# Kernel optimization log

Hardware: AMD Instinct MI355X
Metric: run time of the kernel (lower is better)

## Reference

```python
import jax, jax.numpy as jnp
import numpy as np

N = 100_000      # nodes
E = 1_600_000    # edges (avg degree 16)
IN, H, OUT = 128, 64, 32
G = 128          # graphs in batch
EPS = 1e-5


def setup_inputs() -> dict:
    key = jax.random.key(0)
    ks = jax.random.split(key, 12)
    x = jax.random.normal(ks[0], (N, IN), jnp.float32)
    edge_index = jax.random.randint(ks[1], (2, E), 0, N, dtype=jnp.int32)
    batch = jnp.sort(jax.random.randint(ks[2], (N,), 0, G, dtype=jnp.int32))
    # GCNConv weights (glorot-ish scaling), shared BatchNorm params, final linear
    W1 = jax.random.normal(ks[3], (IN, H), jnp.float32) / np.sqrt(IN)
    b1 = jnp.zeros((H,), jnp.float32)
    W2 = jax.random.normal(ks[4], (H, H), jnp.float32) / np.sqrt(H)
    b2 = jnp.zeros((H,), jnp.float32)
    gamma = jnp.ones((H,), jnp.float32)
    beta = jnp.zeros((H,), jnp.float32)
    linW = jax.random.normal(ks[5], (H, OUT), jnp.float32) / np.sqrt(H)
    linb = jnp.zeros((OUT,), jnp.float32)
    return dict(x=x, edge_index=edge_index, batch=batch, W1=W1, b1=b1,
                W2=W2, b2=b2, gamma=gamma, beta=beta, linW=linW, linb=linb)


def _gcn_edges(edge_index):
    # add self loops (PyG GCNConv default) and symmetric normalization
    loop = jnp.arange(N, dtype=edge_index.dtype)
    src = jnp.concatenate([edge_index[0], loop])
    dst = jnp.concatenate([edge_index[1], loop])
    deg = jax.ops.segment_sum(jnp.ones_like(src, jnp.float32), dst, num_segments=N)
    dis = jnp.where(deg > 0, jax.lax.rsqrt(deg), 0.0)
    norm = dis[src] * dis[dst]          # [E+N]
    return src, dst, norm


def _gcn_conv(h, W, b, src, dst, norm):
    h = h @ W                            # [N, out] small GEMM first (PyG order)
    msg = h[src] * norm[:, None]         # gather + edgewise normalize
    return jax.ops.segment_sum(msg, dst, num_segments=N) + b  # scatter-add


def _batchnorm(h, gamma, beta):
    # training-mode batch stats over nodes (biased variance, as torch BN)
    mean = h.mean(axis=0)
    var = jnp.mean((h - mean) ** 2, axis=0)
    return (h - mean) * jax.lax.rsqrt(var + EPS) * gamma + beta


def reference(x, edge_index, batch, W1, b1, W2, b2, gamma, beta, linW, linb):
    src, dst, norm = _gcn_edges(edge_index)
    h = jax.nn.relu(_batchnorm(_gcn_conv(x, W1, b1, src, dst, norm), gamma, beta))
    h = jax.nn.relu(_batchnorm(_gcn_conv(h, W2, b2, src, dst, norm), gamma, beta))
    # global mean pool over graph ids
    sums = jax.ops.segment_sum(h, batch, num_segments=G)
    cnts = jax.ops.segment_sum(jnp.ones((N,), h.dtype), batch, num_segments=G)
    pooled = sums / jnp.maximum(cnts, 1.0)[:, None]   # [G, H]
    return pooled @ linW + linb                        # [G, OUT]
```

## Files before the change

kernel.cpp:

```cpp
#include <hip/hip_runtime.h>

#define NNODES 100000
#define NEDGES 1600000
#define FIN 128
#define FH 64
#define FOUT 32
#define NGRAPH 128
#define EPSV 1e-5f

#define NBLK ((NNODES + 255) / 256)
#define GM ((NNODES + 63) / 64)
#define FILLBLK 2048
#define POOL_WAVES 1024

typedef unsigned short ushort_t;
typedef __attribute__((ext_vector_type(8))) short bf16x8;
typedef __attribute__((ext_vector_type(4))) float f32x4;

__device__ inline unsigned f2bf(float f) {
  union { float f; unsigned u; } x;
  x.f = f;
  return (x.u + 0x7fffu + ((x.u >> 16) & 1u)) >> 16;
}
__device__ inline float bflo(unsigned u) {
  union { unsigned u; float f; } x;
  x.u = u << 16;
  return x.f;
}
__device__ inline float bfhi(unsigned u) {
  union { unsigned u; float f; } x;
  x.u = u & 0xffff0000u;
  return x.f;
}


__global__ void k_deg_accum(const int* __restrict__ dst, int* __restrict__ deg) {
  const int SLICE = NNODES / 8;
  int xcd = blockIdx.x & 7;
  int lo = xcd * SLICE, hi = lo + SLICE;
  int chunk = blockIdx.x >> 3;
  int nchunk = gridDim.x >> 3;
  for (int i = chunk * blockDim.x + threadIdx.x; i < NEDGES; i += nchunk * blockDim.x) {
    int d = dst[i];
    if (d >= lo && d < hi) atomicAdd(&deg[d], 1);
  }
}


__global__ void k_scan_atomic(const int* __restrict__ deg, int* __restrict__ gtotal,
                              int* __restrict__ off, float* __restrict__ dis) {
  __shared__ int ls[256];
  __shared__ int sbase;
  int b = blockIdx.x, t = threadIdx.x;
  int i = b * 256 + t;
  int v = (i < NNODES) ? deg[i] : 0;
  ls[t] = v;
  __syncthreads();
  for (int s = 1; s < 256; s <<= 1) {
    int add = (t >= s) ? ls[t - s] : 0;
    __syncthreads();
    ls[t] += add;
    __syncthreads();
  }
  if (t == 255) sbase = atomicAdd(gtotal, ls[255]);
  __syncthreads();
  if (i < NNODES) {
    off[i] = sbase + ls[t] - v;
    dis[i] = rsqrtf((float)v + 1.0f);
  }
}


template <int K, bool BN>
__device__ __forceinline__ void gemm_body(int bid, const float* __restrict__ A,
                                          const float* __restrict__ W,
                                          const float* __restrict__ stats,
                                          const float* __restrict__ gamma,
                                          const float* __restrict__ beta,
                                          const float* __restrict__ dis,
                                          ushort_t* __restrict__ out, ushort_t* wt,
                                          float* bn_sc, float* bn_sh) {
  const int WT = K + 8;
  if (BN && threadIdx.x < K) {
    int f = threadIdx.x;
    float mean = stats[f] * (1.0f / NNODES);
    float var = stats[K + f] * (1.0f / NNODES) - mean * mean;
    float s = gamma[f] * rsqrtf(var + EPSV);
    bn_sc[f] = s;
    bn_sh[f] = beta[f] - mean * s;
  }
  for (int idx = threadIdx.x; idx < K * 64; idx += 256) {
    int k = idx >> 6, col = idx & 63;
    wt[col * WT + k] = (ushort_t)f2bf(W[idx]);
  }
  __syncthreads();

  int wave = threadIdx.x >> 6;
  int lane = threadIdx.x & 63;
  int rrow = lane & 15;
  int g = lane >> 4;
  int row0 = (bid * 4 + wave) * 16;
  int arow = min(row0 + rrow, NNODES - 1);
  const float* a = A + (long long)arow * K;

  f32x4 acc0 = {0.f, 0.f, 0.f, 0.f}, acc1 = acc0, acc2 = acc0, acc3 = acc0;

#pragma unroll
  for (int ks = 0; ks < K / 32; ++ks) {
    int koff = ks * 32 + g * 8;
    f32x4 xa = __builtin_nontemporal_load((const f32x4*)(a + koff));
    f32x4 xb = __builtin_nontemporal_load((const f32x4*)(a + koff + 4));
    float xs[8] = {xa.x, xa.y, xa.z, xa.w, xb.x, xb.y, xb.z, xb.w};
    if (BN) {
#pragma unroll
      for (int j = 0; j < 8; ++j)
        xs[j] = fmaxf(fmaf(xs[j], bn_sc[koff + j], bn_sh[koff + j]), 0.0f);
    }
    bf16x8 af;
#pragma unroll
    for (int j = 0; j < 8; ++j) af[j] = (short)f2bf(xs[j]);
    bf16x8 b0 = *(const bf16x8*)&wt[(0 * 16 + rrow) * WT + koff];
    bf16x8 b1 = *(const bf16x8*)&wt[(1 * 16 + rrow) * WT + koff];
    bf16x8 b2 = *(const bf16x8*)&wt[(2 * 16 + rrow) * WT + koff];
    bf16x8 b3 = *(const bf16x8*)&wt[(3 * 16 + rrow) * WT + koff];
    acc0 = __builtin_amdgcn_mfma_f32_16x16x32_bf16(af, b0, acc0, 0, 0, 0);
    acc1 = __builtin_amdgcn_mfma_f32_16x16x32_bf16(af, b1, acc1, 0, 0, 0);
    acc2 = __builtin_amdgcn_mfma_f32_16x16x32_bf16(af, b2, acc2, 0, 0, 0);
    acc3 = __builtin_amdgcn_mfma_f32_16x16x32_bf16(af, b3, acc3, 0, 0, 0);
  }

  int orow0 = row0 + g * 4;
#pragma unroll
  for (int r = 0; r < 4; ++r) {
    int orow = orow0 + r;
    if (orow < NNODES) {
      float d = dis[orow];
      ushort_t* o = out + (long long)orow * FH + rrow;
      o[0] = (ushort_t)f2bf(acc0[r] * d);
      o[16] = (ushort_t)f2bf(acc1[r] * d);
      o[32] = (ushort_t)f2bf(acc2[r] * d);
      o[48] = (ushort_t)f2bf(acc3[r] * d);
    }
  }
}

template <int K, bool BN>
__global__ void k_gemm_mfma(const float* __restrict__ A, const float* __restrict__ W,
                            const float* __restrict__ stats, const float* __restrict__ gamma,
                            const float* __restrict__ beta, const float* __restrict__ dis,
                            ushort_t* __restrict__ out) {
  __shared__ ushort_t wt[64 * (K + 8)];
  __shared__ float sc[K], sh[K];
  gemm_body<K, BN>(blockIdx.x, A, W, stats, gamma, beta, dis, out, wt, sc, sh);
}


__global__ void k_fill_gemm1(const float* __restrict__ x, const float* __restrict__ W1,
                             const float* __restrict__ dis, ushort_t* __restrict__ bufA,
                             const int* __restrict__ src, const int* __restrict__ dst,
                             const int* __restrict__ off, int* __restrict__ cursor,
                             int* __restrict__ csr) {
  __shared__ ushort_t wt[64 * (FIN + 8)];
  if (blockIdx.x < GM) {
    gemm_body<FIN, false>(blockIdx.x, x, W1, nullptr, nullptr, nullptr, dis, bufA, wt,
                          nullptr, nullptr);
  } else {
    int bb = blockIdx.x - GM;
    const int SLICE = NNODES / 8;
    int xcd = bb & 7;
    int lo = xcd * SLICE, hi = lo + SLICE;
    int chunk = bb >> 3;
    int nchunk = FILLBLK >> 3;
    for (int i = chunk * blockDim.x + threadIdx.x; i < NEDGES; i += nchunk * blockDim.x) {
      int d = dst[i];
      if (d >= lo && d < hi) {
        int p = atomicAdd(&cursor[d], 1);
        csr[off[d] + p] = src[i];
      }
    }
  }
}


#define ACC8(acc, u, ok)                       \
  acc[0] += (ok) ? bflo(u.x) : 0.0f;           \
  acc[1] += (ok) ? bfhi(u.x) : 0.0f;           \
  acc[2] += (ok) ? bflo(u.y) : 0.0f;           \
  acc[3] += (ok) ? bfhi(u.y) : 0.0f;           \
  acc[4] += (ok) ? bflo(u.z) : 0.0f;           \
  acc[5] += (ok) ? bfhi(u.z) : 0.0f;           \
  acc[6] += (ok) ? bflo(u.w) : 0.0f;           \
  acc[7] += (ok) ? bfhi(u.w) : 0.0f;

__global__ void k_gather(const ushort_t* __restrict__ hs, const int* __restrict__ csr,
                         const int* __restrict__ off, const int* __restrict__ deg,
                         const float* __restrict__ dis, float* __restrict__ out,
                         float* __restrict__ stats) {
  __shared__ float ls[2 * FH];
  int tid = threadIdx.x;
  if (tid < 2 * FH) ls[tid] = 0.0f;
  __syncthreads();
  int lane = tid & 63;
  int q = lane >> 3;
  int i = lane & 7;
  int wid = (blockIdx.x * blockDim.x + tid) >> 6;
  int nw = (gridDim.x * blockDim.x) >> 6;
  const int HALF = NNODES / 2;
  float s1[8], s2[8];
#pragma unroll
  for (int f = 0; f < 8; ++f) s1[f] = s2[f] = 0.0f;

  for (int p = wid; p < HALF; p += nw) {
    int dA = p, dB = p + HALF;
    int bA = off[dA], eA = bA + deg[dA];
    int bB = off[dB], eB = bB + deg[dB];
    uint4 selfA = *(const uint4*)(hs + (long long)dA * FH + i * 8);
    uint4 selfB = *(const uint4*)(hs + (long long)dB * FH + i * 8);
    float accA[8], accB[8];
#pragma unroll
    for (int f = 0; f < 8; ++f) accA[f] = accB[f] = 0.0f;
    bool q0 = (q == 0);
    ACC8(accA, selfA, q0);
    ACC8(accB, selfB, q0);

    int nA = (eA - bA + 15) >> 4, nB = (eB - bB + 15) >> 4;
    int niter = max(nA, nB);
    int lastA = max(eA - 1, 0), lastB = max(eB - 1, 0);
    int kA0 = bA + q, kA1 = bA + q + 8;
    int kB0 = bB + q, kB1 = bB + q + 8;
    for (int j = 0; j < niter; ++j) {
      int a0 = kA0 + 16 * j, a1 = kA1 + 16 * j;
      int b0 = kB0 + 16 * j, b1 = kB1 + 16 * j;
      int cA0 = csr[min(a0, lastA)];
      int cA1 = csr[min(a1, lastA)];
      int cB0 = csr[min(b0, lastB)];
      int cB1 = csr[min(b1, lastB)];
      uint4 uA0 = *(const uint4*)(hs + (long long)cA0 * FH + i * 8);
      uint4 uA1 = *(const uint4*)(hs + (long long)cA1 * FH + i * 8);
      uint4 uB0 = *(const uint4*)(hs + (long long)cB0 * FH + i * 8);
      uint4 uB1 = *(const uint4*)(hs + (long long)cB1 * FH + i * 8);
      bool A0 = a0 < eA, A1 = a1 < eA, B0 = b0 < eB, B1 = b1 < eB;
      ACC8(accA, uA0, A0);
      ACC8(accA, uA1, A1);
      ACC8(accB, uB0, B0);
      ACC8(accB, uB1, B1);
    }
#pragma unroll
    for (int f = 0; f < 8; ++f) {
      accA[f] += __shfl_xor(accA[f], 8);
      accA[f] += __shfl_xor(accA[f], 16);
      accA[f] += __shfl_xor(accA[f], 32);
      accB[f] += __shfl_xor(accB[f], 8);
      accB[f] += __shfl_xor(accB[f], 16);
      accB[f] += __shfl_xor(accB[f], 32);
    }
    float ddA = dis[dA], ddB = dis[dB];
#pragma unroll
    for (int f = 0; f < 8; ++f) {
      accA[f] *= ddA;
      accB[f] *= ddB;
      s1[f] += accA[f] + accB[f];
      s2[f] += accA[f] * accA[f] + accB[f] * accB[f];
    }
    if (q == 0) {
      f32x4 v0 = {accA[0], accA[1], accA[2], accA[3]};
      f32x4 v1 = {accA[4], accA[5], accA[6], accA[7]};
      *(f32x4*)(out + (long long)dA * FH + i * 8) = v0;
      *(f32x4*)(out + (long long)dA * FH + i * 8 + 4) = v1;
    } else if (q == 1) {
      f32x4 v0 = {accB[0], accB[1], accB[2], accB[3]};
      f32x4 v1 = {accB[4], accB[5], accB[6], accB[7]};
      *(f32x4*)(out + (long long)dB * FH + i * 8) = v0;
      *(f32x4*)(out + (long long)dB * FH + i * 8 + 4) = v1;
    }
  }
  if (q == 2) {
#pragma unroll
    for (int f = 0; f < 8; ++f) {
      atomicAdd(&ls[i * 8 + f], s1[f]);
      atomicAdd(&ls[FH + i * 8 + f], s2[f]);
    }
  }
  __syncthreads();
  if (tid < 2 * FH) atomicAdd(&stats[tid], ls[tid]);
}


__global__ void k_pool(const float* __restrict__ h, const int* __restrict__ batch,
                       const float* __restrict__ stats, const float* __restrict__ gamma,
                       const float* __restrict__ beta, float* __restrict__ pooled,
                       float* __restrict__ cnt) {
  const int CHUNK = (NNODES + POOL_WAVES - 1) / POOL_WAVES;
  int lane = threadIdx.x & 63;
  int wid = (blockIdx.x * blockDim.x + threadIdx.x) >> 6;
  int start = wid * CHUNK;
  if (start >= NNODES) return;
  int end = min(start + CHUNK, NNODES);
  float mean = stats[lane] * (1.0f / NNODES);
  float var = stats[FH + lane] * (1.0f / NNODES) - mean * mean;
  float sc = gamma[lane] * rsqrtf(var + EPSV);
  float sh = beta[lane] - mean * sc;
  int cur = batch[start];
  float acc = 0.0f;
  int cl = 0;
  for (int n = start; n < end; ++n) {
    int g = batch[n];
    if (g != cur) {
      atomicAdd(&pooled[cur * FH + lane], acc);
      if (lane == 0) atomicAdd(&cnt[cur], (float)cl);
      acc = 0.0f;
      cl = 0;
      cur = g;
    }
    float v = fmaf(h[(long long)n * FH + lane], sc, sh);
    acc += fmaxf(v, 0.0f);
    ++cl;
  }
  atomicAdd(&pooled[cur * FH + lane], acc);
  if (lane == 0) atomicAdd(&cnt[cur], (float)cl);
}


__global__ void k_final(const float* __restrict__ pooled, const float* __restrict__ cnt,
                        const float* __restrict__ linW, const float* __restrict__ linb,
                        float* __restrict__ out) {
  int t = blockIdx.x * blockDim.x + threadIdx.x;
  if (t >= NGRAPH * FOUT) return;
  int g = t / FOUT, o = t % FOUT;
  float inv = 1.0f / fmaxf(cnt[g], 1.0f);
  float acc = linb[o];
#pragma unroll
  for (int k = 0; k < FH; ++k) acc = fmaf(pooled[g * FH + k] * inv, linW[k * FOUT + o], acc);
  out[t] = acc;
}

extern "C" void kernel_launch(void* const* d_in, const int* in_sizes, int n_in,
                              void* d_out, int out_size, void* d_ws, size_t ws_size,
                              hipStream_t stream) {
  const float* x = (const float*)d_in[0];
  const int* esrc = (const int*)d_in[1];
  const int* edst = (const int*)d_in[1] + NEDGES;
  const int* batch = (const int*)d_in[2];
  const float* W1 = (const float*)d_in[3];
  const float* W2 = (const float*)d_in[5];
  const float* gamma = (const float*)d_in[7];
  const float* beta = (const float*)d_in[8];
  const float* linW = (const float*)d_in[9];
  const float* linb = (const float*)d_in[10];
  float* out = (float*)d_out;

  ushort_t* bufA = (ushort_t*)d_ws;
  float* bufB = (float*)(bufA + (long long)NNODES * FH);
  float* dis = bufB + (long long)NNODES * FH;
  int* off = (int*)(dis + NNODES);
  int* csr = off + NNODES;
  int* deg = csr + NEDGES;
  int* cursor = deg + NNODES;
  int* gtotal = cursor + NNODES;
  float* stats1 = (float*)(gtotal + 1);
  float* stats2 = stats1 + 2 * FH;
  float* pooled = stats2 + 2 * FH;
  float* cnt = pooled + NGRAPH * FH;

  const int BT = 256;

  hipMemsetAsync(deg, 0,
                 (size_t)(2 * NNODES + 1 + 2 * 2 * FH + NGRAPH * FH + NGRAPH) * sizeof(int),
                 stream);

  k_deg_accum<<<2048, BT, 0, stream>>>(edst, deg);
  k_scan_atomic<<<NBLK, BT, 0, stream>>>(deg, gtotal, off, dis);
  k_fill_gemm1<<<GM + FILLBLK, BT, 0, stream>>>(x, W1, dis, bufA, esrc, edst, off, cursor, csr);

  k_gather<<<2048, BT, 0, stream>>>(bufA, csr, off, deg, dis, bufB, stats1);

  k_gemm_mfma<FH, true><<<GM, BT, 0, stream>>>(bufB, W2, stats1, gamma, beta, dis, bufA);
  k_gather<<<2048, BT, 0, stream>>>(bufA, csr, off, deg, dis, bufB, stats2);

  k_pool<<<POOL_WAVES * 64 / BT, BT, 0, stream>>>(bufB, batch, stats2, gamma, beta, pooled, cnt);
  k_final<<<(NGRAPH * FOUT + BT - 1) / BT, BT, 0, stream>>>(pooled, cnt, linW, linb, out);
}
```

Baseline: 432.0 us.

## Fuse mean pooling and final linear into one per-graph kernel

Replaces the atomic chunked pooling kernel and the separate final linear kernel with one kernel that launches one block per graph. Each block binary-searches the sorted batch array for its node range, reduces in shared memory and applies the linear layer. This removes one launch, the global atomics and part of the memset. The cost is only 128 blocks of 4 waves each, which may underuse the GPU while streaming the node features.

```diff
diff --git a/kernel.cpp b/kernel.cpp
--- a/kernel.cpp
+++ b/kernel.cpp
@@ -11,7 +11,6 @@
 #define NBLK ((NNODES + 255) / 256)
 #define GM ((NNODES + 63) / 64)
 #define FILLBLK 2048
-#define POOL_WAVES 1024
 
 typedef unsigned short ushort_t;
 typedef __attribute__((ext_vector_type(8))) short bf16x8;
@@ -286,52 +285,52 @@
 }
 
 
-__global__ void k_pool(const float* __restrict__ h, const int* __restrict__ batch,
-                       const float* __restrict__ stats, const float* __restrict__ gamma,
-                       const float* __restrict__ beta, float* __restrict__ pooled,
-                       float* __restrict__ cnt) {
-  const int CHUNK = (NNODES + POOL_WAVES - 1) / POOL_WAVES;
-  int lane = threadIdx.x & 63;
-  int wid = (blockIdx.x * blockDim.x + threadIdx.x) >> 6;
-  int start = wid * CHUNK;
-  if (start >= NNODES) return;
-  int end = min(start + CHUNK, NNODES);
+__global__ void k_pool_final(const float* __restrict__ h, const int* __restrict__ batch,
+                             const float* __restrict__ stats, const float* __restrict__ gamma,
+                             const float* __restrict__ beta, const float* __restrict__ linW,
+                             const float* __restrict__ linb, float* __restrict__ out) {
+  __shared__ int srange[2];
+  __shared__ float partial[4][FH];
+  __shared__ float pooledv[FH];
+  int g = blockIdx.x;
+  int tid = threadIdx.x;
+  if (tid < 2) {
+    int target = g + tid;
+    int lo = 0, hi = NNODES;
+    while (lo < hi) {
+      int mid = (lo + hi) >> 1;
+      if (batch[mid] < target) lo = mid + 1;
+      else hi = mid;
+    }
+    srange[tid] = lo;
+  }
+  __syncthreads();
+  int start = srange[0], end = srange[1];
+  int lane = tid & 63;
+  int wave = tid >> 6;
   float mean = stats[lane] * (1.0f / NNODES);
   float var = stats[FH + lane] * (1.0f / NNODES) - mean * mean;
   float sc = gamma[lane] * rsqrtf(var + EPSV);
   float sh = beta[lane] - mean * sc;
-  int cur = batch[start];
   float acc = 0.0f;
-  int cl = 0;
-  for (int n = start; n < end; ++n) {
-    int g = batch[n];
-    if (g != cur) {
-      atomicAdd(&pooled[cur * FH + lane], acc);
-      if (lane == 0) atomicAdd(&cnt[cur], (float)cl);
-      acc = 0.0f;
-      cl = 0;
-      cur = g;
-    }
+  for (int n = start + wave; n < end; n += 4) {
     float v = fmaf(h[(long long)n * FH + lane], sc, sh);
     acc += fmaxf(v, 0.0f);
-    ++cl;
-  }
-  atomicAdd(&pooled[cur * FH + lane], acc);
-  if (lane == 0) atomicAdd(&cnt[cur], (float)cl);
-}
-
-
-__global__ void k_final(const float* __restrict__ pooled, const float* __restrict__ cnt,
-                        const float* __restrict__ linW, const float* __restrict__ linb,
-                        float* __restrict__ out) {
-  int t = blockIdx.x * blockDim.x + threadIdx.x;
-  if (t >= NGRAPH * FOUT) return;
-  int g = t / FOUT, o = t % FOUT;
-  float inv = 1.0f / fmaxf(cnt[g], 1.0f);
-  float acc = linb[o];
-#pragma unroll
-  for (int k = 0; k < FH; ++k) acc = fmaf(pooled[g * FH + k] * inv, linW[k * FOUT + o], acc);
-  out[t] = acc;
+  }
+  partial[wave][lane] = acc;
+  __syncthreads();
+  if (tid < FH) {
+    float inv = 1.0f / fmaxf((float)(end - start), 1.0f);
+    pooledv[tid] =
+        (partial[0][tid] + partial[1][tid] + partial[2][tid] + partial[3][tid]) * inv;
+  }
+  __syncthreads();
+  if (tid < FOUT) {
+    float acc2 = linb[tid];
+#pragma unroll
+    for (int k = 0; k < FH; ++k) acc2 = fmaf(pooledv[k], linW[k * FOUT + tid], acc2);
+    out[g * FOUT + tid] = acc2;
+  }
 }
 
 extern "C" void kernel_launch(void* const* d_in, const int* in_sizes, int n_in,
@@ -359,14 +358,10 @@
   int* gtotal = cursor + NNODES;
   float* stats1 = (float*)(gtotal + 1);
   float* stats2 = stats1 + 2 * FH;
-  float* pooled = stats2 + 2 * FH;
-  float* cnt = pooled + NGRAPH * FH;
 
   const int BT = 256;
 
-  hipMemsetAsync(deg, 0,
-                 (size_t)(2 * NNODES + 1 + 2 * 2 * FH + NGRAPH * FH + NGRAPH) * sizeof(int),
-                 stream);
+  hipMemsetAsync(deg, 0, (size_t)(2 * NNODES + 1 + 2 * 2 * FH) * sizeof(int), stream);
 
   k_deg_accum<<<2048, BT, 0, stream>>>(edst, deg);
   k_scan_atomic<<<NBLK, BT, 0, stream>>>(deg, gtotal, off, dis);
@@ -377,6 +372,5 @@
   k_gemm_mfma<FH, true><<<GM, BT, 0, stream>>>(bufB, W2, stats1, gamma, beta, dis, bufA);
   k_gather<<<2048, BT, 0, stream>>>(bufA, csr, off, deg, dis, bufB, stats2);
 
-  k_pool<<<POOL_WAVES * 64 / BT, BT, 0, stream>>>(bufB, batch, stats2, gamma, beta, pooled, cnt);
-  k_final<<<(NGRAPH * FOUT + BT - 1) / BT, BT, 0, stream>>>(pooled, cnt, linW, linb, out);
-}
+  k_pool_final<<<NGRAPH, BT, 0, stream>>>(bufB, batch, stats2, gamma, beta, linW, linb, out);
+}
```

After: 452.8 us. 4.8% more time.
